# Optimization experiments

Hardware: AMD Instinct MI355X
Metric: run time of the kernel (lower is better)

## Reference

```python
import jax, jax.numpy as jnp
import numpy as np

N = 50000
E = 800000
DIMS = [128, 256, 64, 256, 128]  # encoder 128->256->64, decoder 64->256->128
NEG_SLOPE = 0.01


def setup_inputs() -> dict:
    key = jax.random.key(0)
    keys = jax.random.split(key, 2 + 3 * 4)
    inp = {
        "x": jax.random.normal(keys[0], (N, DIMS[0]), dtype=jnp.float32),
        "edge_index": jax.random.randint(keys[1], (2, E), 0, N, dtype=jnp.int64),
    }
    for i in range(4):
        d_in, d_out = DIMS[i], DIMS[i + 1]
        s = 1.0 / np.sqrt(d_in)
        inp[f"W_rel{i}"] = jax.random.uniform(keys[2 + 3 * i], (d_out, d_in), jnp.float32, -s, s)
        inp[f"W_root{i}"] = jax.random.uniform(keys[3 + 3 * i], (d_out, d_in), jnp.float32, -s, s)
        inp[f"b{i}"] = jax.random.uniform(keys[4 + 3 * i], (d_out,), jnp.float32, -s, s)
    return inp


def graph_conv(x, edge_index, W_rel, W_root, b):
    # PyG GraphConv: lin_rel(sum_{j->i} x_j) + lin_root(x_i), bias in lin_rel
    src, dst = edge_index[0], edge_index[1]
    agg = jax.ops.segment_sum(x[src], dst, num_segments=N)  # [N, d_in]
    return agg @ W_rel.T + b + x @ W_root.T


def reference(x, edge_index,
              W_rel0, W_root0, b0, W_rel1, W_root1, b1,
              W_rel2, W_root2, b2, W_rel3, W_root3, b3):
    params = [(W_rel0, W_root0, b0), (W_rel1, W_root1, b1),
              (W_rel2, W_root2, b2), (W_rel3, W_root3, b3)]
    h = x
    emb = None
    for i, (Wr, Ws, b) in enumerate(params):
        h = graph_conv(h, edge_index, Wr, Ws, b)
        h = jax.nn.leaky_relu(h, negative_slope=NEG_SLOPE)
        if i == 1:  # end of encoder -> embedding
            emb = h
    return h, emb
```

## Files before the change

kernel.cpp:

```cpp
#include <hip/hip_runtime.h>

#define NNODES 50000
#define NCB 196

typedef __attribute__((ext_vector_type(8))) short bf16x8;
typedef __attribute__((ext_vector_type(4))) float f32x4;

__device__ inline short f2bf(float f) {
    unsigned u = __float_as_uint(f);
    unsigned r = (u + 0x7FFFu + ((u >> 16) & 1u)) >> 16;
    return (short)r;
}
__device__ inline float bf2f(short s) {
    return __uint_as_float(((unsigned)(unsigned short)s) << 16);
}
__device__ inline float2 bfp2f(int p) {
    float2 f;
    f.x = __uint_as_float((unsigned)p << 16);
    f.y = __uint_as_float((unsigned)p & 0xFFFF0000u);
    return f;
}
__device__ inline void addbf4(float4& a, int2 v) {
    float2 lo = bfp2f(v.x), hi = bfp2f(v.y);
    a.x += lo.x; a.y += lo.y; a.z += hi.x; a.w += hi.y;
}
__device__ inline void addbf8(float* a, int4 v) {
    float2 l0 = bfp2f(v.x), l1 = bfp2f(v.y), l2 = bfp2f(v.z), l3 = bfp2f(v.w);
    a[0] += l0.x; a[1] += l0.y; a[2] += l1.x; a[3] += l1.y;
    a[4] += l2.x; a[5] += l2.y; a[6] += l3.x; a[7] += l3.y;
}
__device__ inline int pack2(float a, float b) {
    return ((int)(unsigned short)f2bf(a)) | ((int)f2bf(b) << 16);
}

__device__ inline int excl_scan_256(int v, int* lds, int tid) {
    int lane = tid & 63, w = tid >> 6;
    int incl = v;
    #pragma unroll
    for (int off = 1; off < 64; off <<= 1) {
        int t = __shfl_up(incl, off, 64);
        if (lane >= off) incl += t;
    }
    if (lane == 63) lds[w] = incl;
    __syncthreads();
    if (tid == 0) {
        int s = 0;
        #pragma unroll
        for (int i = 0; i < 4; i++) { int t = lds[i]; lds[i] = s; s += t; }
    }
    __syncthreads();
    return incl - v + lds[w];
}

__global__ __launch_bounds__(256) void hist_coarse(
    const int* __restrict__ dst, int* __restrict__ histG, int E, int chunk)
{
    __shared__ int h[NCB];
    const int tid = threadIdx.x;
    for (int i = tid; i < NCB; i += 256) h[i] = 0;
    __syncthreads();
    const int beg = blockIdx.x * chunk;
    const int end = min(beg + chunk, E);
    for (int e = beg + tid; e < end; e += 256)
        atomicAdd(&h[dst[e] >> 8], 1);
    __syncthreads();
    for (int i = tid; i < NCB; i += 256)
        histG[i * 256 + blockIdx.x] = h[i];
}

__global__ __launch_bounds__(256) void scan_buckets(
    int* __restrict__ histG, int* __restrict__ btot)
{
    __shared__ int lds[8];
    const int tid = threadIdx.x;
    const int b = blockIdx.x;
    int v = histG[b * 256 + tid];
    int ex = excl_scan_256(v, lds, tid);
    histG[b * 256 + tid] = ex;
    if (tid == 255) btot[b] = ex + v;
}

__global__ __launch_bounds__(256) void scan_bases(
    const int* __restrict__ btot, int* __restrict__ bases, int E)
{
    __shared__ int lds[8];
    const int tid = threadIdx.x;
    int v = (tid < NCB) ? btot[tid] : 0;
    int ex = excl_scan_256(v, lds, tid);
    if (tid <= NCB) bases[tid] = ex;
}

__global__ __launch_bounds__(256) void scatter_coarse(
    const int* __restrict__ src, const int* __restrict__ dst,
    const int* __restrict__ histG, const int* __restrict__ bases,
    int* __restrict__ coarse, int E, int chunk)
{
    __shared__ int pos[NCB];
    const int tid = threadIdx.x;
    const int blk = blockIdx.x;
    for (int i = tid; i < NCB; i += 256)
        pos[i] = bases[i] + histG[i * 256 + blk];
    __syncthreads();
    const int beg = blk * chunk;
    const int end = min(beg + chunk, E);
    for (int e = beg + tid; e < end; e += 256) {
        int d = dst[e];
        int p = atomicAdd(&pos[d >> 8], 1);
        coarse[p] = ((d & 255) << 16) | src[e];
    }
}

__global__ __launch_bounds__(256) void fill_from_coarse(
    const int* __restrict__ bases, const int* __restrict__ coarse,
    int* __restrict__ rowptr, int* __restrict__ col, int N)
{
    __shared__ int hist[256], rp[256], pos[256];
    __shared__ int lds[8];
    const int cb  = blockIdx.x;
    const int tid = threadIdx.x;
    const int n0  = cb << 8;
    const int beg = bases[cb], end = bases[cb + 1];
    hist[tid] = 0; pos[tid] = 0;
    __syncthreads();
    for (int e = beg + tid; e < end; e += 256)
        atomicAdd(&hist[coarse[e] >> 16], 1);
    __syncthreads();
    int ex = excl_scan_256(hist[tid], lds, tid);
    rp[tid] = beg + ex;
    if (n0 + tid <= N) rowptr[n0 + tid] = beg + ex;
    __syncthreads();
    for (int e = beg + tid; e < end; e += 256) {
        int pk = coarse[e];
        int dl = pk >> 16;
        int p = atomicAdd(&pos[dl], 1);
        col[rp[dl] + p] = pk & 0xFFFF;
    }
}

__global__ __launch_bounds__(256) void cvt_x(const float* __restrict__ in,
                                             short* __restrict__ out, int n4) {
    int i = blockIdx.x * 256 + threadIdx.x;
    if (i < n4) {
        float4 v = ((const float4*)in)[i];
        short4 s;
        s.x = f2bf(v.x); s.y = f2bf(v.y); s.z = f2bf(v.z); s.w = f2bf(v.w);
        *(short4*)(out + (size_t)i * 4) = s;
    }
}

__global__ __launch_bounds__(256) void cvt_weights(
    const float* __restrict__ p0, const float* __restrict__ p1,
    const float* __restrict__ p2, const float* __restrict__ p3,
    const float* __restrict__ p4, const float* __restrict__ p5,
    const float* __restrict__ p6, const float* __restrict__ p7,
    short* __restrict__ out) {
    int g = blockIdx.x * 256 + threadIdx.x;
    if (g >= 196608) return;
    const float* src; int off;
    if      (g <  32768) { src = p0; off = g; }
    else if (g <  65536) { src = p1; off = g -  32768; }
    else if (g <  81920) { src = p2; off = g -  65536; }
    else if (g <  98304) { src = p3; off = g -  81920; }
    else if (g < 114688) { src = p4; off = g -  98304; }
    else if (g < 131072) { src = p5; off = g - 114688; }
    else if (g < 163840) { src = p6; off = g - 131072; }
    else                 { src = p7; off = g - 163840; }
    out[g] = f2bf(src[off]);
}

__global__ __launch_bounds__(256) void gather_sum128(
    const short* __restrict__ xbf, const int* __restrict__ rowptr,
    const int* __restrict__ col, short* __restrict__ aggbf, int N)
{
    const int wave = threadIdx.x >> 6;
    const int lane = threadIdx.x & 63;
    const int node = blockIdx.x * 4 + wave;
    if (node >= N) return;
    const int g = lane >> 4;
    const int c = lane & 15;
    const int beg = rowptr[node], end = rowptr[node + 1];
    float acc[8] = {};
    const int last = end - 1;
    for (int e = beg; e < end; e += 16) {
        const int e0 = e + g, e1 = e + 4 + g, e2 = e + 8 + g, e3 = e + 12 + g;
        const bool m0 = e0 < end, m1 = e1 < end, m2 = e2 < end, m3 = e3 < end;
        const int i0 = col[min(e0, last)];
        const int i1 = col[min(e1, last)];
        const int i2 = col[min(e2, last)];
        const int i3 = col[min(e3, last)];
        int4 v0 = *(const int4*)(xbf + (size_t)i0 * 128 + c * 8);
        int4 v1 = *(const int4*)(xbf + (size_t)i1 * 128 + c * 8);
        int4 v2 = *(const int4*)(xbf + (size_t)i2 * 128 + c * 8);
        int4 v3 = *(const int4*)(xbf + (size_t)i3 * 128 + c * 8);
        if (m0) addbf8(acc, v0);
        if (m1) addbf8(acc, v1);
        if (m2) addbf8(acc, v2);
        if (m3) addbf8(acc, v3);
    }
    #pragma unroll
    for (int k = 0; k < 8; k++) acc[k] += __shfl_down(acc[k], 32);
    #pragma unroll
    for (int k = 0; k < 8; k++) acc[k] += __shfl_down(acc[k], 16);
    if (g == 0) {
        int4 sv;
        sv.x = pack2(acc[0], acc[1]);
        sv.y = pack2(acc[2], acc[3]);
        sv.z = pack2(acc[4], acc[5]);
        sv.w = pack2(acc[6], acc[7]);
        *(int4*)(aggbf + (size_t)node * 128 + c * 8) = sv;
    }
}

__global__ __launch_bounds__(256) void gather_sum64(
    const short* __restrict__ xbf, const int* __restrict__ rowptr,
    const int* __restrict__ col, short* __restrict__ aggbf, int N)
{
    const int wave = threadIdx.x >> 6;
    const int lane = threadIdx.x & 63;
    const int node = blockIdx.x * 4 + wave;
    if (node >= N) return;
    const int g = lane >> 3;
    const int c = lane & 7;
    const int beg = rowptr[node], end = rowptr[node + 1];
    float acc[8] = {};
    const int last = end - 1;
    for (int e = beg; e < end; e += 16) {
        const int e0 = e + g, e1 = e + 8 + g;
        const bool m0 = e0 < end, m1 = e1 < end;
        const int i0 = col[min(e0, last)];
        const int i1 = col[min(e1, last)];
        int4 v0 = *(const int4*)(xbf + (size_t)i0 * 64 + c * 8);
        int4 v1 = *(const int4*)(xbf + (size_t)i1 * 64 + c * 8);
        if (m0) addbf8(acc, v0);
        if (m1) addbf8(acc, v1);
    }
    #pragma unroll
    for (int k = 0; k < 8; k++) acc[k] += __shfl_down(acc[k], 32);
    #pragma unroll
    for (int k = 0; k < 8; k++) acc[k] += __shfl_down(acc[k], 16);
    #pragma unroll
    for (int k = 0; k < 8; k++) acc[k] += __shfl_down(acc[k], 8);
    if (g == 0) {
        int4 sv;
        sv.x = pack2(acc[0], acc[1]);
        sv.y = pack2(acc[2], acc[3]);
        sv.z = pack2(acc[4], acc[5]);
        sv.w = pack2(acc[6], acc[7]);
        *(int4*)(aggbf + (size_t)node * 64 + c * 8) = sv;
    }
}

__global__ __launch_bounds__(256) void gather_fin128(
    const short* __restrict__ zw, const int* __restrict__ rowptr,
    const int* __restrict__ col, const float* __restrict__ bias,
    float* __restrict__ out, int N)
{
    const int wave = threadIdx.x >> 6;
    const int lane = threadIdx.x & 63;
    const int node = blockIdx.x * 4 + wave;
    if (node >= N) return;
    const int g = lane >> 4;
    const int c = lane & 15;
    const int beg = rowptr[node], end = rowptr[node + 1];
    float acc[8] = {};
    if (g == 0) {
        int4 wv = *(const int4*)(zw + (size_t)node * 256 + 128 + c * 8);
        addbf8(acc, wv);
        float4 b0 = *(const float4*)(bias + c * 8);
        float4 b1 = *(const float4*)(bias + c * 8 + 4);
        acc[0] += b0.x; acc[1] += b0.y; acc[2] += b0.z; acc[3] += b0.w;
        acc[4] += b1.x; acc[5] += b1.y; acc[6] += b1.z; acc[7] += b1.w;
    }
    const int last = end - 1;
    for (int e = beg; e < end; e += 16) {
        const int e0 = e + g, e1 = e + 4 + g, e2 = e + 8 + g, e3 = e + 12 + g;
        const bool m0 = e0 < end, m1 = e1 < end, m2 = e2 < end, m3 = e3 < end;
        const int i0 = col[min(e0, last)];
        const int i1 = col[min(e1, last)];
        const int i2 = col[min(e2, last)];
        const int i3 = col[min(e3, last)];
        int4 v0 = *(const int4*)(zw + (size_t)i0 * 256 + c * 8);
        int4 v1 = *(const int4*)(zw + (size_t)i1 * 256 + c * 8);
        int4 v2 = *(const int4*)(zw + (size_t)i2 * 256 + c * 8);
        int4 v3 = *(const int4*)(zw + (size_t)i3 * 256 + c * 8);
        if (m0) addbf8(acc, v0);
        if (m1) addbf8(acc, v1);
        if (m2) addbf8(acc, v2);
        if (m3) addbf8(acc, v3);
    }
    #pragma unroll
    for (int k = 0; k < 8; k++) acc[k] += __shfl_down(acc[k], 32);
    #pragma unroll
    for (int k = 0; k < 8; k++) acc[k] += __shfl_down(acc[k], 16);
    if (g == 0) {
        #pragma unroll
        for (int k = 0; k < 8; k++) acc[k] = acc[k] > 0.f ? acc[k] : 0.01f * acc[k];
        float4 o0 = make_float4(acc[0], acc[1], acc[2], acc[3]);
        float4 o1 = make_float4(acc[4], acc[5], acc[6], acc[7]);
        *(float4*)(out + (size_t)node * 128 + c * 8)     = o0;
        *(float4*)(out + (size_t)node * 128 + c * 8 + 4) = o1;
    }
}

__global__ __launch_bounds__(256) void gather_fin64(
    const short* __restrict__ zw, const int* __restrict__ rowptr,
    const int* __restrict__ col, const float* __restrict__ bias,
    float* __restrict__ out, short* __restrict__ out_bf, int N)
{
    const int wave = threadIdx.x >> 6;
    const int lane = threadIdx.x & 63;
    const int node = blockIdx.x * 4 + wave;
    if (node >= N) return;
    const int g = lane >> 3;
    const int c = lane & 7;
    const int beg = rowptr[node], end = rowptr[node + 1];
    float acc[8] = {};
    if (g == 0) {
        int4 wv = *(const int4*)(zw + (size_t)node * 128 + 64 + c * 8);
        addbf8(acc, wv);
        float4 b0 = *(const float4*)(bias + c * 8);
        float4 b1 = *(const float4*)(bias + c * 8 + 4);
        acc[0] += b0.x; acc[1] += b0.y; acc[2] += b0.z; acc[3] += b0.w;
        acc[4] += b1.x; acc[5] += b1.y; acc[6] += b1.z; acc[7] += b1.w;
    }
    const int last = end - 1;
    for (int e = beg; e < end; e += 16) {
        const int e0 = e + g, e1 = e + 8 + g;
        const bool m0 = e0 < end, m1 = e1 < end;
        const int i0 = col[min(e0, last)];
        const int i1 = col[min(e1, last)];
        int4 v0 = *(const int4*)(zw + (size_t)i0 * 128 + c * 8);
        int4 v1 = *(const int4*)(zw + (size_t)i1 * 128 + c * 8);
        if (m0) addbf8(acc, v0);
        if (m1) addbf8(acc, v1);
    }
    #pragma unroll
    for (int k = 0; k < 8; k++) acc[k] += __shfl_down(acc[k], 32);
    #pragma unroll
    for (int k = 0; k < 8; k++) acc[k] += __shfl_down(acc[k], 16);
    #pragma unroll
    for (int k = 0; k < 8; k++) acc[k] += __shfl_down(acc[k], 8);
    if (g == 0) {
        #pragma unroll
        for (int k = 0; k < 8; k++) acc[k] = acc[k] > 0.f ? acc[k] : 0.01f * acc[k];
        float4 o0 = make_float4(acc[0], acc[1], acc[2], acc[3]);
        float4 o1 = make_float4(acc[4], acc[5], acc[6], acc[7]);
        *(float4*)(out + (size_t)node * 64 + c * 8)     = o0;
        *(float4*)(out + (size_t)node * 64 + c * 8 + 4) = o1;
        int4 sv;
        sv.x = pack2(acc[0], acc[1]);
        sv.y = pack2(acc[2], acc[3]);
        sv.z = pack2(acc[4], acc[5]);
        sv.w = pack2(acc[6], acc[7]);
        *(int4*)(out_bf + (size_t)node * 64 + c * 8) = sv;
    }
}

template<int DK, int DOUT, bool FUSED>
__global__ __launch_bounds__(256, 4) void gemm_mfma(
    const short* __restrict__ A0, const short* __restrict__ A1,
    const short* __restrict__ B0, const short* __restrict__ B1,
    const float* __restrict__ bias, short* __restrict__ outH, int N)
{
    constexpr int KTOT  = FUSED ? 2 * DK : DK;
    constexpr int NCOLS = FUSED ? DOUT : 2 * DOUT;
    constexpr int K32   = KTOT / 32;

    __shared__ short eps[4 * 4608];
    const int tid  = threadIdx.x;
    const int row0 = blockIdx.x * 128;
    const int col0 = blockIdx.y * 128;
    const int w    = tid >> 6;
    const int lane = tid & 63;
    const int wr   = (w & 1) << 6;
    const int wc   = (w >> 1) << 6;
    const int m16  = lane & 15;
    const int quad = lane >> 4;

    const short* arow[4];
    #pragma unroll
    for (int i = 0; i < 4; i++) {
        int r = row0 + wr + i * 16 + m16;
        r = r < N ? r : N - 1;
        arow[i] = A0 + (size_t)r * DK + (quad << 3);
    }
    const size_t a1d = FUSED ? (size_t)(A1 - A0) : 0;

    const short* blo[4];
    const short* bhi[4];
    #pragma unroll
    for (int j = 0; j < 4; j++) {
        const int cg = col0 + wc + j * 16 + m16;
        if (FUSED) {
            blo[j] = B0 + (size_t)cg * DK + (quad << 3);
            bhi[j] = B1 + (size_t)cg * DK + (quad << 3);
        } else {
            blo[j] = ((cg < DOUT) ? (B0 + (size_t)cg * DK)
                                  : (B1 + (size_t)(cg - DOUT) * DK)) + (quad << 3);
            bhi[j] = blo[j];
        }
    }

    f32x4 acc[4][4] = {};

    #pragma unroll
    for (int kk = 0; kk < K32; kk++) {
        const int ko = kk * 32;
        bf16x8 af[4];
        #pragma unroll
        for (int i = 0; i < 4; i++) {
            const short* ap = arow[i];
            if (FUSED && ko >= DK) ap += a1d + (ko - DK);
            else                   ap += ko;
            af[i] = *(const bf16x8*)ap;
        }
        #pragma unroll
        for (int j = 0; j < 4; j++) {
            const short* bp;
            if (FUSED && ko >= DK) bp = bhi[j] + (ko - DK);
            else                   bp = blo[j] + ko;
            bf16x8 bfr = *(const bf16x8*)bp;
            #pragma unroll
            for (int i = 0; i < 4; i++)
                acc[i][j] = __builtin_amdgcn_mfma_f32_16x16x32_bf16(
                    bfr, af[i], acc[i][j], 0, 0, 0);
        }
    }

    short* ep = eps + w * 4608;
    #pragma unroll
    for (int j = 0; j < 4; j++) {
        const int cb = wc + j * 16 + (quad << 2);
        float4 bv = make_float4(0.f, 0.f, 0.f, 0.f);
        if (FUSED) bv = *(const float4*)(bias + col0 + cb);
        #pragma unroll
        for (int i = 0; i < 4; i++) {
            float v0 = acc[i][j][0], v1 = acc[i][j][1];
            float v2 = acc[i][j][2], v3 = acc[i][j][3];
            if (FUSED) {
                v0 += bv.x; v1 += bv.y; v2 += bv.z; v3 += bv.w;
                v0 = v0 > 0.f ? v0 : 0.01f * v0;
                v1 = v1 > 0.f ? v1 : 0.01f * v1;
                v2 = v2 > 0.f ? v2 : 0.01f * v2;
                v3 = v3 > 0.f ? v3 : 0.01f * v3;
            }
            int2 pv;
            pv.x = pack2(v0, v1);
            pv.y = pack2(v2, v3);
            *(int2*)(ep + (i * 16 + m16) * 72 + j * 16 + (quad << 2)) = pv;
        }
    }
    const int r8  = lane >> 3;
    const int seg = lane & 7;
    #pragma unroll
    for (int rb = 0; rb < 8; rb++) {
        const int lrow = rb * 8 + r8;
        int4 vv = *(const int4*)(ep + lrow * 72 + seg * 8);
        const int grow = row0 + wr + lrow;
        if (grow < N)
            *(int4*)(outH + (size_t)grow * NCOLS + col0 + wc + seg * 8) = vv;
    }
}

extern "C" void kernel_launch(void* const* d_in, const int* in_sizes, int n_in,
                              void* d_out, int out_size, void* d_ws, size_t ws_size,
                              hipStream_t stream) {
    const int N = NNODES;
    const float* x  = (const float*)d_in[0];
    const int*   ei = (const int*)d_in[1];
    const int    E  = in_sizes[1] / 2;
    const int* src = ei;
    const int* dst = ei + E;

    const float* Wr[4] = { (const float*)d_in[2], (const float*)d_in[5],
                           (const float*)d_in[8], (const float*)d_in[11] };
    const float* Ws[4] = { (const float*)d_in[3], (const float*)d_in[6],
                           (const float*)d_in[9], (const float*)d_in[12] };
    const float* bb[4] = { (const float*)d_in[4], (const float*)d_in[7],
                           (const float*)d_in[10], (const float*)d_in[13] };

    float* out  = (float*)d_out;
    float* emb  = out + (size_t)N * 128;

    short* zwbf   = (short*)d_ws;
    short* aggbf  = zwbf + (size_t)N * 256;
    short* xbf    = aggbf + (size_t)N * 128;
    short* h1bf   = xbf + (size_t)N * 128;
    short* embbf  = h1bf + (size_t)N * 256;
    short* wbf    = embbf + (size_t)N * 64;
    int*   rowptr = (int*)(wbf + 196608);
    int*   col    = rowptr + (N + 1);
    int*   coarse = col + E;
    int*   histG  = coarse + E;
    int*   btot   = histG + NCB * 256;
    int*   bases  = btot + NCB;

    const short* wr0 = wbf;           const short* ws0 = wbf + 32768;
    const short* wr1 = wbf + 65536;   const short* ws1 = wbf + 81920;
    const short* wr2 = wbf + 98304;   const short* ws2 = wbf + 114688;
    const short* wr3 = wbf + 131072;  const short* ws3 = wbf + 163840;

    const int chunk = (E + 255) / 256;
    const int gemmRB = (N + 127) / 128;
    const int nodeBlocks = (N + 3) / 4;

    hist_coarse<<<256, 256, 0, stream>>>(dst, histG, E, chunk);
    scan_buckets<<<NCB, 256, 0, stream>>>(histG, btot);
    scan_bases<<<1, 256, 0, stream>>>(btot, bases, E);
    scatter_coarse<<<256, 256, 0, stream>>>(src, dst, histG, bases, coarse, E, chunk);
    fill_from_coarse<<<NCB, 256, 0, stream>>>(bases, coarse, rowptr, col, N);
    cvt_x<<<(N * 128 / 4 + 255) / 256, 256, 0, stream>>>(x, xbf, N * 128 / 4);
    cvt_weights<<<(196608 + 255) / 256, 256, 0, stream>>>(
        Wr[0], Ws[0], Wr[1], Ws[1], Wr[2], Ws[2], Wr[3], Ws[3], wbf);

    gather_sum128<<<nodeBlocks, 256, 0, stream>>>(xbf, rowptr, col, aggbf, N);
    gemm_mfma<128, 256, true><<<dim3(gemmRB, 2), 256, 0, stream>>>(
        aggbf, xbf, wr0, ws0, bb[0], h1bf, N);

    gemm_mfma<256, 64, false><<<dim3(gemmRB, 1), 256, 0, stream>>>(
        h1bf, nullptr, wr1, ws1, nullptr, zwbf, N);
    gather_fin64<<<nodeBlocks, 256, 0, stream>>>(
        zwbf, rowptr, col, bb[1], emb, embbf, N);

    gather_sum64<<<nodeBlocks, 256, 0, stream>>>(embbf, rowptr, col, aggbf, N);
    gemm_mfma<64, 256, true><<<dim3(gemmRB, 2), 256, 0, stream>>>(
        aggbf, embbf, wr2, ws2, bb[2], h1bf , N);

    gemm_mfma<256, 128, false><<<dim3(gemmRB, 2), 256, 0, stream>>>(
        h1bf , nullptr, wr3, ws3, nullptr, zwbf, N);
    gather_fin128<<<nodeBlocks, 256, 0, stream>>>(
        zwbf, rowptr, col, bb[3], out, N);
}
```

Before: 359.6 us.

## Stage GEMM weight tile in LDS via direct global-to-LDS loads, 256-row blocks

The MFMA GEMM now preloads the block's full 128-column weight slice into shared memory with global_load_lds, in fragment order, and reads B fragments from LDS instead of global memory. The block grows to 512 threads covering 256 rows, so each staged weight tile serves twice as many rows and global weight reads per output drop. The cost is a larger shared-memory footprint (up to 64KB for K=256), a barrier before compute, and fewer resident blocks. The epilogue reuses the same LDS buffer after an added sync.

```diff
diff --git a/kernel.cpp b/kernel.cpp
--- a/kernel.cpp
+++ b/kernel.cpp
@@ -5,6 +5,9 @@
 
 typedef __attribute__((ext_vector_type(8))) short bf16x8;
 typedef __attribute__((ext_vector_type(4))) float f32x4;
+
+#define AS1 __attribute__((address_space(1)))
+#define AS3 __attribute__((address_space(3)))
 
 __device__ inline short f2bf(float f) {
     unsigned u = __float_as_uint(f);
@@ -357,7 +360,7 @@
 }
 
 template<int DK, int DOUT, bool FUSED>
-__global__ __launch_bounds__(256, 4) void gemm_mfma(
+__global__ __launch_bounds__(512, 2) void gemm_mfma(
     const short* __restrict__ A0, const short* __restrict__ A1,
     const short* __restrict__ B0, const short* __restrict__ B1,
     const float* __restrict__ bias, short* __restrict__ outH, int N)
@@ -365,17 +368,45 @@
     constexpr int KTOT  = FUSED ? 2 * DK : DK;
     constexpr int NCOLS = FUSED ? DOUT : 2 * DOUT;
     constexpr int K32   = KTOT / 32;
-
-    __shared__ short eps[4 * 4608];
+    constexpr int LOG2K32 = (K32 == 8) ? 3 : 2;
+    constexpr int BSH   = 128 * KTOT;
+    constexpr int BI4   = BSH / 8;
+    constexpr int ITER  = BI4 / 512;
+    constexpr int EPSH  = 8 * 4608;
+    constexpr int SMSH  = (BSH > EPSH) ? BSH : EPSH;
+
+    __shared__ short smem[SMSH];
     const int tid  = threadIdx.x;
-    const int row0 = blockIdx.x * 128;
+    const int row0 = blockIdx.x * 256;
     const int col0 = blockIdx.y * 128;
     const int w    = tid >> 6;
     const int lane = tid & 63;
-    const int wr   = (w & 1) << 6;
-    const int wc   = (w >> 1) << 6;
+    const int wr   = (w & 3) << 6;
+    const int wc   = (w >> 2) << 6;
     const int m16  = lane & 15;
     const int quad = lane >> 4;
+
+    #pragma unroll
+    for (int it = 0; it < ITER; it++) {
+        const int L  = tid + it * 512;
+        const int mm = L & 15;
+        const int qd = (L >> 4) & 3;
+        const int kk = (L >> 6) & (K32 - 1);
+        const int jj = L >> (6 + LOG2K32);
+        const int j  = col0 + jj * 16 + mm;
+        const int ko = (kk * 4 + qd) * 8;
+        const short* bp;
+        if (FUSED) {
+            if (ko < DK) bp = B0 + (size_t)j * DK + ko;
+            else         bp = B1 + (size_t)j * DK + (ko - DK);
+        } else {
+            bp = (j < DOUT) ? (B0 + (size_t)j * DK + ko)
+                            : (B1 + (size_t)(j - DOUT) * DK + ko);
+        }
+        __builtin_amdgcn_global_load_lds(
+            (const AS1 void*)bp, (AS3 void*)(smem + ((size_t)L << 3)), 16, 0, 0);
+    }
+    __syncthreads();
 
     const short* arow[4];
     #pragma unroll
@@ -386,22 +417,8 @@
     }
     const size_t a1d = FUSED ? (size_t)(A1 - A0) : 0;
 
-    const short* blo[4];
-    const short* bhi[4];
-    #pragma unroll
-    for (int j = 0; j < 4; j++) {
-        const int cg = col0 + wc + j * 16 + m16;
-        if (FUSED) {
-            blo[j] = B0 + (size_t)cg * DK + (quad << 3);
-            bhi[j] = B1 + (size_t)cg * DK + (quad << 3);
-        } else {
-            blo[j] = ((cg < DOUT) ? (B0 + (size_t)cg * DK)
-                                  : (B1 + (size_t)(cg - DOUT) * DK)) + (quad << 3);
-            bhi[j] = blo[j];
-        }
-    }
-
     f32x4 acc[4][4] = {};
+    const int jw = wc >> 4;
 
     #pragma unroll
     for (int kk = 0; kk < K32; kk++) {
@@ -416,10 +433,8 @@
         }
         #pragma unroll
         for (int j = 0; j < 4; j++) {
-            const short* bp;
-            if (FUSED && ko >= DK) bp = bhi[j] + (ko - DK);
-            else                   bp = blo[j] + ko;
-            bf16x8 bfr = *(const bf16x8*)bp;
+            bf16x8 bfr = *(const bf16x8*)(smem +
+                (((((jw + j) * K32 + kk) * 4 + quad) * 16 + m16) << 3));
             #pragma unroll
             for (int i = 0; i < 4; i++)
                 acc[i][j] = __builtin_amdgcn_mfma_f32_16x16x32_bf16(
@@ -427,7 +442,9 @@
         }
     }
 
-    short* ep = eps + w * 4608;
+    __syncthreads();
+
+    short* ep = smem + w * 4608;
     #pragma unroll
     for (int j = 0; j < 4; j++) {
         const int cb = wc + j * 16 + (quad << 2);
@@ -501,7 +518,7 @@
     const short* wr3 = wbf + 131072;  const short* ws3 = wbf + 163840;
 
     const int chunk = (E + 255) / 256;
-    const int gemmRB = (N + 127) / 128;
+    const int gemmRB = (N + 255) / 256;
     const int nodeBlocks = (N + 3) / 4;
 
     hist_coarse<<<256, 256, 0, stream>>>(dst, histG, E, chunk);
@@ -514,19 +531,19 @@
         Wr[0], Ws[0], Wr[1], Ws[1], Wr[2], Ws[2], Wr[3], Ws[3], wbf);
 
     gather_sum128<<<nodeBlocks, 256, 0, stream>>>(xbf, rowptr, col, aggbf, N);
-    gemm_mfma<128, 256, true><<<dim3(gemmRB, 2), 256, 0, stream>>>(
+    gemm_mfma<128, 256, true><<<dim3(gemmRB, 2), 512, 0, stream>>>(
         aggbf, xbf, wr0, ws0, bb[0], h1bf, N);
 
-    gemm_mfma<256, 64, false><<<dim3(gemmRB, 1), 256, 0, stream>>>(
+    gemm_mfma<256, 64, false><<<dim3(gemmRB, 1), 512, 0, stream>>>(
         h1bf, nullptr, wr1, ws1, nullptr, zwbf, N);
     gather_fin64<<<nodeBlocks, 256, 0, stream>>>(
         zwbf, rowptr, col, bb[1], emb, embbf, N);
 
     gather_sum64<<<nodeBlocks, 256, 0, stream>>>(embbf, rowptr, col, aggbf, N);
-    gemm_mfma<64, 256, true><<<dim3(gemmRB, 2), 256, 0, stream>>>(
+    gemm_mfma<64, 256, true><<<dim3(gemmRB, 2), 512, 0, stream>>>(
         aggbf, embbf, wr2, ws2, bb[2], h1bf , N);
 
-    gemm_mfma<256, 128, false><<<dim3(gemmRB, 2), 256, 0, stream>>>(
+    gemm_mfma<256, 128, false><<<dim3(gemmRB, 2), 512, 0, stream>>>(
         h1bf , nullptr, wr3, ws3, nullptr, zwbf, N);
     gather_fin128<<<nodeBlocks, 256, 0, stream>>>(
         zwbf, rowptr, col, bb[3], out, N);
```

Result: faster. 324.0 us (-9.9%).
